# Performance work log

Measured on AMD Instinct MI355X. Metric: run time of the kernel, lower is better.

The kernel has to match this reference:

```python
import jax, jax.numpy as jnp
import numpy as np

B, T = 262144, 512


def setup_inputs() -> dict:
    key = jax.random.key(0)
    k1, k2, k3 = jax.random.split(key, 3)
    # per-row sub-probability distribution so logs stay finite (matches model assumption)
    p = jax.random.uniform(k1, (B, T), jnp.float32, minval=1e-3, maxval=1.0)
    y_pred = p / (jnp.sum(p, axis=1, keepdims=True) * 1.01)
    y = jax.random.randint(k2, (B,), 0, T)
    status = jax.random.randint(k3, (B,), 0, 2)
    return {"y_pred": y_pred, "y": y, "status": status}


def reference(y_pred, y, status):
    # Vectorized equivalent of the per-sample python loop:
    #  status==1: -log(y_pred[i, y[i]])
    #  status==0: -log(1 - sum(y_pred[i, :y[i]]))  (exclusive prefix sum)
    csum = jnp.cumsum(y_pred, axis=1)                     # [B, T]
    rows = jnp.arange(y_pred.shape[0])
    p_v = y_pred[rows, y]                                 # y_pred[i, v]
    ex_sum = jnp.where(y > 0, csum[rows, jnp.maximum(y - 1, 0)], 0.0)  # sum y_pred[i,:v]
    per_sample = jnp.where(status == 1, -jnp.log(p_v), -jnp.log(1.0 - ex_sum))
    return jnp.sum(per_sample)
```

## Files before the change

### kernel.cpp

```cpp
#include <hip/hip_runtime.h>

#define TDIM 512

__global__ __launch_bounds__(256) void surv_loss_kernel(
    const float* __restrict__ y_pred,
    const int* __restrict__ y,
    const int* __restrict__ status,
    float* __restrict__ out,
    unsigned char* __restrict__ ws,
    int nrows) {
  double* acc = reinterpret_cast<double*>(ws);
  unsigned int* counter = reinterpret_cast<unsigned int*>(ws + 8);

  const int lane = threadIdx.x & 63;
  const int widb = threadIdx.x >> 6;
  const int gwave = blockIdx.x * 4 + widb;
  const int nwaves = gridDim.x * 4;

  float wacc = 0.0f;

  for (int row = gwave; row < nrows; row += nwaves) {
    const int v = y[row];
    const int st = status[row];
    const float* rowp = y_pred + (size_t)row * TDIM;

    if (st == 1) {
      if (lane == 0) wacc -= logf(rowp[v]);
    } else {
      float s = 0.0f;
      {
        const int e0 = lane * 4;
        if (e0 < v) {
          float4 d = *reinterpret_cast<const float4*>(rowp + e0);
          s += d.x;
          if (e0 + 1 < v) s += d.y;
          if (e0 + 2 < v) s += d.z;
          if (e0 + 3 < v) s += d.w;
        }
      }
      {
        const int e1 = 256 + lane * 4;
        if (e1 < v) {
          float4 d = *reinterpret_cast<const float4*>(rowp + e1);
          s += d.x;
          if (e1 + 1 < v) s += d.y;
          if (e1 + 2 < v) s += d.z;
          if (e1 + 3 < v) s += d.w;
        }
      }
      #pragma unroll
      for (int off = 32; off >= 1; off >>= 1) s += __shfl_xor(s, off, 64);
      if (lane == 0) wacc -= logf(1.0f - s);
    }
  }

  __shared__ float sm[4];
  if (lane == 0) sm[widb] = wacc;
  __syncthreads();
  if (threadIdx.x == 0) {
    float bsum = sm[0] + sm[1] + sm[2] + sm[3];
    atomicAdd(acc, (double)bsum);
    __threadfence();
    unsigned int old = atomicAdd(counter, 1u);
    if (old == gridDim.x - 1) {
      __threadfence();
      double total = atomicAdd(acc, 0.0);
      out[0] = (float)total;
    }
  }
}

extern "C" void kernel_launch(void* const* d_in, const int* in_sizes, int n_in,
                              void* d_out, int out_size, void* d_ws, size_t ws_size,
                              hipStream_t stream) {
  const float* y_pred = (const float*)d_in[0];
  const int* y = (const int*)d_in[1];
  const int* status = (const int*)d_in[2];
  float* out = (float*)d_out;
  const int nrows = in_sizes[1];

  hipMemsetAsync(d_ws, 0, 16, stream);

  const int grid = 2048;
  surv_loss_kernel<<<grid, 256, 0, stream>>>(y_pred, y, status, out,
                                             (unsigned char*)d_ws, nrows);
}
```

Measured before the change: 676.7 us.

## Process 8 rows per wave with batched metadata loads and sharded atomics

Each wave now handles a fixed block of 32 rows. It loads y and status for all 32 rows at once, one row per lane. Prefix sums are computed with 8 lanes per row, so 8 rows run concurrently and only a 3-step shuffle reduction is needed instead of a full wave reduction. The grid becomes one block per 128 rows rather than a grid-stride loop, and the double accumulator is spread over 64 slots so the final atomics contend less. The intent is more memory-level parallelism and less serialized per-row latency, at the cost of many more blocks and more unrolled loads per lane.

Result: no change. 681.1 us (+0.7%).

```diff
diff --git a/kernel.cpp b/kernel.cpp
--- a/kernel.cpp
+++ b/kernel.cpp
@@ -1,6 +1,10 @@
 #include <hip/hip_runtime.h>
 
 #define TDIM 512
+#define ROWS_PER_WAVE 32
+#define WAVES_PER_BLOCK 4
+#define ROWS_PER_BLOCK (ROWS_PER_WAVE * WAVES_PER_BLOCK)
+#define NSLOTS 64
 
 __global__ __launch_bounds__(256) void surv_loss_kernel(
     const float* __restrict__ y_pred,
@@ -8,65 +12,81 @@
     const int* __restrict__ status,
     float* __restrict__ out,
     unsigned char* __restrict__ ws,
-    int nrows) {
+    int nrows, int nblocks) {
   double* acc = reinterpret_cast<double*>(ws);
-  unsigned int* counter = reinterpret_cast<unsigned int*>(ws + 8);
+  unsigned int* counter = reinterpret_cast<unsigned int*>(ws + NSLOTS * 8);
 
   const int lane = threadIdx.x & 63;
   const int widb = threadIdx.x >> 6;
-  const int gwave = blockIdx.x * 4 + widb;
-  const int nwaves = gridDim.x * 4;
+  const int gwave = blockIdx.x * WAVES_PER_BLOCK + widb;
+  const long r0 = (long)gwave * ROWS_PER_WAVE;
 
-  float wacc = 0.0f;
+  float lacc = 0.0f;
 
-  for (int row = gwave; row < nrows; row += nwaves) {
-    const int v = y[row];
-    const int st = status[row];
+  const int lrow = (int)r0 + (lane & 31);
+  const bool lvalid = lrow < nrows;
+  const int lclamp = lvalid ? lrow : (nrows - 1);
+  const int v_l = y[lclamp];
+  const int st_l = status[lclamp];
+
+  {
+    const bool g = (lane < 32) && lvalid && (st_l == 1);
+    float pv = 1.0f;
+    if (g) pv = y_pred[(size_t)lclamp * TDIM + v_l];
+    if (g) lacc -= logf(pv);
+  }
+
+  const int g8 = lane >> 3;
+  const int t8 = lane & 7;
+  #pragma unroll
+  for (int b = 0; b < 4; ++b) {
+    const int k = b * 8 + g8;
+    const int vk = __shfl(v_l, k, 64);
+    const int stk = __shfl(st_l, k, 64);
+    const long row = r0 + k;
+    const bool rvalid = (row < (long)nrows) && (stk == 0);
+    const int ve = rvalid ? vk : 0;
     const float* rowp = y_pred + (size_t)row * TDIM;
 
-    if (st == 1) {
-      if (lane == 0) wacc -= logf(rowp[v]);
-    } else {
-      float s = 0.0f;
-      {
-        const int e0 = lane * 4;
-        if (e0 < v) {
-          float4 d = *reinterpret_cast<const float4*>(rowp + e0);
-          s += d.x;
-          if (e0 + 1 < v) s += d.y;
-          if (e0 + 2 < v) s += d.z;
-          if (e0 + 3 < v) s += d.w;
-        }
+    float s = 0.0f;
+    #pragma unroll
+    for (int p = 0; p < 16; ++p) {
+      const int e = p * 32 + t8 * 4;
+      if (e < ve) {
+        float4 d = *reinterpret_cast<const float4*>(rowp + e);
+        s += d.x;
+        if (e + 1 < ve) s += d.y;
+        if (e + 2 < ve) s += d.z;
+        if (e + 3 < ve) s += d.w;
       }
-      {
-        const int e1 = 256 + lane * 4;
-        if (e1 < v) {
-          float4 d = *reinterpret_cast<const float4*>(rowp + e1);
-          s += d.x;
-          if (e1 + 1 < v) s += d.y;
-          if (e1 + 2 < v) s += d.z;
-          if (e1 + 3 < v) s += d.w;
-        }
-      }
-      #pragma unroll
-      for (int off = 32; off >= 1; off >>= 1) s += __shfl_xor(s, off, 64);
-      if (lane == 0) wacc -= logf(1.0f - s);
     }
+    s += __shfl_xor(s, 1, 64);
+    s += __shfl_xor(s, 2, 64);
+    s += __shfl_xor(s, 4, 64);
+    if (rvalid && t8 == 0) lacc -= logf(1.0f - s);
   }
 
-  __shared__ float sm[4];
-  if (lane == 0) sm[widb] = wacc;
+  #pragma unroll
+  for (int off = 32; off >= 1; off >>= 1) lacc += __shfl_xor(lacc, off, 64);
+
+  __shared__ float sm[WAVES_PER_BLOCK];
+  __shared__ int is_last;
+  if (lane == 0) sm[widb] = lacc;
   __syncthreads();
   if (threadIdx.x == 0) {
-    float bsum = sm[0] + sm[1] + sm[2] + sm[3];
-    atomicAdd(acc, (double)bsum);
+    const float bsum = sm[0] + sm[1] + sm[2] + sm[3];
+    atomicAdd(&acc[blockIdx.x & (NSLOTS - 1)], (double)bsum);
     __threadfence();
-    unsigned int old = atomicAdd(counter, 1u);
-    if (old == gridDim.x - 1) {
-      __threadfence();
-      double total = atomicAdd(acc, 0.0);
-      out[0] = (float)total;
-    }
+    const unsigned int old = atomicAdd(counter, 1u);
+    is_last = (old == (unsigned int)(nblocks - 1)) ? 1 : 0;
+  }
+  __syncthreads();
+
+  if (is_last && threadIdx.x < NSLOTS) {
+    double myv = atomicAdd(&acc[threadIdx.x], 0.0);
+    #pragma unroll
+    for (int off = 32; off >= 1; off >>= 1) myv += __shfl_xor(myv, off, 64);
+    if (threadIdx.x == 0) out[0] = (float)myv;
   }
 }
 
@@ -79,9 +99,9 @@
   float* out = (float*)d_out;
   const int nrows = in_sizes[1];
 
-  hipMemsetAsync(d_ws, 0, 16, stream);
+  hipMemsetAsync(d_ws, 0, NSLOTS * 8 + 8, stream);
 
-  const int grid = 2048;
-  surv_loss_kernel<<<grid, 256, 0, stream>>>(y_pred, y, status, out,
-                                             (unsigned char*)d_ws, nrows);
+  const int nblocks = (nrows + ROWS_PER_BLOCK - 1) / ROWS_PER_BLOCK;
+  surv_loss_kernel<<<nblocks, 256, 0, stream>>>(y_pred, y, status, out,
+                                                (unsigned char*)d_ws, nrows, nblocks);
 }
```
